# Kernel optimization log

Measured on AMD Instinct MI355X. Metric: run time of the kernel, lower is better.

The kernel has to match this reference:

```python
import jax, jax.numpy as jnp
import numpy as np

K = 16            # k_neighbors
THRESH = 0.5      # edge weight threshold
COS_EPS = 1e-8
LN_EPS = 1e-5


def setup_inputs() -> dict:
    key = jax.random.key(0)
    ks = jax.random.split(key, 8)
    B, L, D, H, O = 4, 2048, 64, 128, 64
    def w(k, shape, fan_in):
        return jax.random.normal(k, shape, jnp.float32) / np.float32(np.sqrt(fan_in))
    return {
        "x":  jax.random.normal(ks[0], (B, L, D), jnp.float32),
        "W1": w(ks[1], (D, H), D), "b1": jnp.zeros((H,), jnp.float32),
        "g1": jnp.ones((H,), jnp.float32), "be1": jnp.zeros((H,), jnp.float32),
        "W2": w(ks[2], (H, O), H), "b2": jnp.zeros((O,), jnp.float32),
        "g2": jnp.ones((O,), jnp.float32), "be2": jnp.zeros((O,), jnp.float32),
        "Wp": w(ks[3], (O, D), O), "bp": jnp.zeros((D,), jnp.float32),
    }


def _layer_norm(x, g, b):
    mu = x.mean(-1, keepdims=True)
    var = ((x - mu) ** 2).mean(-1, keepdims=True)
    return (x - mu) * jax.lax.rsqrt(var + LN_EPS) * g + b


def _gcn_layer(x, src, dst, ew, W, b, g, beta, N):
    # PyG GCNConv with gcn_norm(add_self_loops=True): append one more
    # weight-1.0 self loop per node, then symmetric deg^-1/2 normalization.
    ar = jnp.arange(N)
    src2 = jnp.concatenate([src, ar])
    dst2 = jnp.concatenate([dst, ar])
    w2 = jnp.concatenate([ew, jnp.ones((N,), x.dtype)])
    deg = jax.ops.segment_sum(w2, dst2, num_segments=N)           # [N]
    dinv = jnp.where(deg > 0, jax.lax.rsqrt(jnp.where(deg > 0, deg, 1.0)), 0.0)
    norm = dinv[src2] * w2 * dinv[dst2]                           # [E']
    h = x @ W                                                     # [N, out]
    out = jax.ops.segment_sum(norm[:, None] * h[src2], dst2, num_segments=N) + b
    out = jax.nn.relu(out)        # activation (dropout = eval identity)
    return _layer_norm(out, g, beta)


def _build_graph(xf, N):
    # cosine similarity (dense N x N), top-(K+1) per row, drop self (col 0),
    # zero out edges below threshold (equivalent to removing them for GCN),
    # then add constructor self loops with weight 1.0.
    nrm = jnp.linalg.norm(xf, axis=1)
    sim = (xf @ xf.T) / (nrm[:, None] * nrm[None, :] + COS_EPS)   # [N, N]
    vals, idx = jax.lax.top_k(sim, K + 1)
    src = jnp.repeat(jnp.arange(N), K)
    dst = idx[:, 1:].reshape(-1)
    wv = vals[:, 1:].reshape(-1)
    wv = jnp.where(wv > THRESH, wv, 0.0)
    ar = jnp.arange(N)
    edge_src = jnp.concatenate([src, ar])
    edge_dst = jnp.concatenate([dst, ar])
    # original detaches weights via .item(): stop_gradient to match
    edge_w = jax.lax.stop_gradient(
        jnp.concatenate([wv, jnp.ones((N,), xf.dtype)]))
    return edge_src, edge_dst, edge_w


def reference(x, W1, b1, g1, be1, W2, b2, g2, be2, Wp, bp):
    B, L, D = x.shape
    N = B * L
    xf = x.reshape(N, D)
    src, dst, ew = _build_graph(xf, N)
    h = _gcn_layer(xf, src, dst, ew, W1, b1, g1, be1, N)
    h = _gcn_layer(h,  src, dst, ew, W2, b2, g2, be2, N)
    out = (h @ Wp + bp).reshape(B, L, D)
    edge_index = jnp.stack([src, dst])
    return out, edge_index, ew
```

## Files before the change

kernel.cpp:

```cpp
#include <hip/hip_runtime.h>
#include <cstdint>
#include <climits>

#define N 8192
#define D 64
#define H 128
#define O 64
#define KNB 16
#define NE (N*KNB)
#define ETOT (NE + N)
#define OUT0 (N*D)
#define NSPL 32
#define JSPAN 256
#define JTILE 128
#define TCH 8

__device__ __forceinline__ float bf2f(unsigned short u){
    union { unsigned int u; float f; } v; v.u = ((unsigned int)u) << 16; return v.f;
}
__device__ __forceinline__ unsigned short f2bf(float f){
    union { float f; unsigned int u; } v; v.f = f;
    unsigned int r = v.u + 0x7FFFu + ((v.u >> 16) & 1u);
    return (unsigned short)(r >> 16);
}

#define PIN4(v) asm volatile("" : "+v"((v).x), "+v"((v).y), "+v"((v).z), "+v"((v).w))

__global__ void k_probe(const unsigned short* __restrict__ x, int* __restrict__ flag){
    __shared__ int cnt;
    if (threadIdx.x == 0) cnt = 0;
    __syncthreads();
    unsigned short u = x[2*threadIdx.x];
    int e = (u >> 7) & 0xFF;
    int ok = (u == 0) || (e >= 0x60 && e <= 0x85);
    unsigned long long m = __ballot(ok);
    if ((threadIdx.x & 63) == 0) atomicAdd(&cnt, __popcll(m));
    __syncthreads();
    if (threadIdx.x == 0) *flag = (cnt >= 128) ? 1 : 0;
}

__global__ void k_cvt(const void* __restrict__ src, float* __restrict__ dst,
                      int n, const int* __restrict__ flag){
    int i = blockIdx.x*256 + threadIdx.x;
    if (i >= n) return;
    if (*flag) dst[i] = bf2f(((const unsigned short*)src)[i]);
    else       dst[i] = ((const float*)src)[i];
}

__global__ void k_cvtp(const void* s1, const void* s2, const void* s3, const void* s4,
                       const void* s5, const void* s6, const void* s7, const void* s8,
                       const void* s9, const void* s10,
                       float* d1, float* d2, float* d3, float* d4, float* d5,
                       float* d6, float* d7, float* d8, float* d9, float* d10,
                       const int* __restrict__ flag){
    int id = blockIdx.x*256 + threadIdx.x;
    const void* s; float* d; int off;
    if      (id <  8192){ s = s1;  d = d1;  off = id; }
    else if (id <  8320){ s = s2;  d = d2;  off = id - 8192; }
    else if (id <  8448){ s = s3;  d = d3;  off = id - 8320; }
    else if (id <  8576){ s = s4;  d = d4;  off = id - 8448; }
    else if (id < 16768){ s = s5;  d = d5;  off = id - 8576; }
    else if (id < 16832){ s = s6;  d = d6;  off = id - 16768; }
    else if (id < 16896){ s = s7;  d = d7;  off = id - 16832; }
    else if (id < 16960){ s = s8;  d = d8;  off = id - 16896; }
    else if (id < 21056){ s = s9;  d = d9;  off = id - 16960; }
    else if (id < 21120){ s = s10; d = d10; off = id - 21056; }
    else return;
    if (*flag) d[off] = bf2f(((const unsigned short*)s)[off]);
    else       d[off] = ((const float*)s)[off];
}

__global__ void k_prep(const float* __restrict__ xf, float* __restrict__ nrmf){
    int i = blockIdx.x*64 + threadIdx.x;
    const float* xr = xf + i*D;
    float r[8];
    #pragma unroll
    for (int q = 0; q < 8; ++q) r[q] = __fmul_rn(xr[q], xr[q]);
    #pragma unroll
    for (int b = 8; b < 64; b += 8)
        #pragma unroll
        for (int q = 0; q < 8; ++q)
            r[q] = __fadd_rn(r[q], __fmul_rn(xr[b+q], xr[b+q]));
    float s = __fadd_rn(__fadd_rn(__fadd_rn(r[0],r[1]), __fadd_rn(r[2],r[3])),
                        __fadd_rn(__fadd_rn(r[4],r[5]), __fadd_rn(r[6],r[7])));
    nrmf[i] = __fsqrt_rn(s);
}


__global__ __launch_bounds__(256, 2) void k_scan8(const float* __restrict__ xf,
                                                  const float* __restrict__ nrmf,
                                                  float* __restrict__ chV,
                                                  int* __restrict__ chI){
    __shared__ float sB[JTILE*64];
    __shared__ float sN[JTILE];

    int tid = threadIdx.x;
    int grp = blockIdx.x & 31;
    int split = blockIdx.x >> 5;
    int i = grp*256 + tid;
    int jbase = split*JSPAN;

    const float4* xip = (const float4*)(xf + (size_t)i*D);
    float4 xi4[16];
    #pragma unroll
    for (int c = 0; c < 16; ++c) xi4[c] = xip[c];
    #pragma unroll
    for (int c = 0; c < 16; ++c) PIN4(xi4[c]);
    float ni = nrmf[i];

    float lv[TCH]; int li[TCH];
    #pragma unroll
    for (int r = 0; r < TCH; ++r){ lv[r] = -3.0e38f; li[r] = INT_MAX; }

    for (int t = 0; t < JSPAN/JTILE; ++t){
        int jt = jbase + t*JTILE;
        __syncthreads();
        #pragma unroll
        for (int u = 0; u < (JTILE*16)/256; ++u){
            int idx = u*256 + tid;
            ((float4*)sB)[idx] = ((const float4*)xf)[(size_t)jt*16 + idx];
        }
        if (tid < JTILE) sN[tid] = nrmf[jt + tid];
        __syncthreads();

        for (int jj = 0; jj < JTILE; ++jj){
            int j = jt + jj;
            const float4* B4 = (const float4*)(sB + jj*64);
            float nj = sN[jj];
            float a = 0.0f;
            #pragma unroll
            for (int c = 0; c < 16; ++c){
                float4 b = B4[c]; float4 xa = xi4[c];
                a = __fmaf_rn(b.x, xa.x, a);
                a = __fmaf_rn(b.y, xa.y, a);
                a = __fmaf_rn(b.z, xa.z, a);
                a = __fmaf_rn(b.w, xa.w, a);
            }
            float den = __fadd_rn(__fmul_rn(ni, nj), 1e-8f);
            float thr = lv[TCH-1]*den;
            if (j != i && a > __fmaf_rn(fabsf(thr), -1e-6f, thr)){
                float s0 = __fdiv_rn(a, den);
                if (s0 > lv[TCH-1]){
                    lv[TCH-1] = s0; li[TCH-1] = j;
                    #pragma unroll
                    for (int r = TCH-1; r > 0; --r){
                        if (lv[r] > lv[r-1]){
                            float tv = lv[r]; lv[r] = lv[r-1]; lv[r-1] = tv;
                            int ti = li[r]; li[r] = li[r-1]; li[r-1] = ti;
                        }
                    }
                }
            }
        }
    }
    #pragma unroll
    for (int r = 0; r < TCH; ++r){
        chV[(size_t)(split*TCH + r)*N + i] = lv[r];
        chI[(size_t)(split*TCH + r)*N + i] = li[r];
    }
}

__global__ __launch_bounds__(256, 2) void k_sel16(const float* __restrict__ xf,
                                                  const float* __restrict__ nrmf,
                                                  const float* __restrict__ chV,
                                                  const int* __restrict__ chI,
                                                  int* __restrict__ topIdx,
                                                  float* __restrict__ ewArr){
    int q = (blockIdx.x*256 + threadIdx.x) >> 6;
    int lane = threadIdx.x & 63;

    unsigned long long okey[4], key[4];
    #pragma unroll
    for (int s = 0; s < 4; ++s){
        int slot = lane + 64*s;
        float v = chV[(size_t)slot*N + q];
        int  id = chI[(size_t)slot*N + q];
        unsigned int u = __float_as_uint(v);
        if ((u & 0x7FFFFFFFu) == 0u) u = 0u;
        u = (u & 0x80000000u) ? ~u : (u | 0x80000000u);
        unsigned long long kk = ((unsigned long long)u << 32)
                              | (unsigned long long)(unsigned int)(~(unsigned int)id);
        okey[s] = kk; key[s] = kk;
    }

    float wv[16]; int widx[16];
    unsigned long long k16 = 0ull;
    #pragma unroll
    for (int sel = 0; sel < KNB; ++sel){
        unsigned long long m = key[0] > key[1] ? key[0] : key[1];
        if (key[2] > m) m = key[2];
        if (key[3] > m) m = key[3];
        #pragma unroll
        for (int off = 32; off > 0; off >>= 1){
            unsigned long long o = __shfl_xor(m, off);
            if (o > m) m = o;
        }
        if      (key[0] == m) key[0] = 0ull;
        else if (key[1] == m) key[1] = 0ull;
        else if (key[2] == m) key[2] = 0ull;
        else if (key[3] == m) key[3] = 0ull;
        unsigned int um = (unsigned int)(m >> 32);
        unsigned int ou = (um & 0x80000000u) ? (um & 0x7FFFFFFFu) : ~um;
        wv[sel]  = __uint_as_float(ou);
        widx[sel] = (int)~((unsigned int)m);
        k16 = m;
    }

    bool fl = false;
    #pragma unroll
    for (int s = 0; s < 4; ++s){
        int slot = lane + 64*s;
        if ((slot % TCH) == TCH-1 && okey[s] > k16) fl = true;
    }
    if (__ballot(fl) == 0ull){
        if (lane == 0){
            #pragma unroll
            for (int sel = 0; sel < KNB; ++sel){
                topIdx[q*KNB + sel] = widx[sel];
                ewArr [q*KNB + sel] = (wv[sel] > 0.5f) ? wv[sel] : 0.0f;
            }
        }
        return;
    }
    if (lane != 0) return;

    float lv[16]; int li[16];
    #pragma unroll
    for (int r = 0; r < 16; ++r){ lv[r] = -3.0e38f; li[r] = INT_MAX; }
    unsigned int flags = 0;
    for (int c = 0; c < NSPL; ++c){
        float v8 = chV[(size_t)(c*TCH + TCH-1)*N + q];
        int  i8 = chI[(size_t)(c*TCH + TCH-1)*N + q];
        if (v8 > wv[15] || (v8 == wv[15] && i8 < widx[15])) flags |= (1u << c);
    }
    const float4* xq4 = (const float4*)(xf + (size_t)q*D);
    float4 xq[16];
    #pragma unroll
    for (int c = 0; c < 16; ++c) xq[c] = xq4[c];
    float ni = nrmf[q];
    for (int c = 0; c < NSPL; ++c){
        if ((flags >> c) & 1u){
            for (int j = c*JSPAN; j < c*JSPAN + JSPAN; ++j){
                if (j == q) continue;
                const float4* b4 = (const float4*)(xf + (size_t)j*D);
                float a = 0.0f;
                #pragma unroll
                for (int k = 0; k < 16; ++k){
                    float4 b = b4[k]; float4 xa = xq[k];
                    a = __fmaf_rn(b.x, xa.x, a);
                    a = __fmaf_rn(b.y, xa.y, a);
                    a = __fmaf_rn(b.z, xa.z, a);
                    a = __fmaf_rn(b.w, xa.w, a);
                }
                float den = __fadd_rn(__fmul_rn(ni, nrmf[j]), 1e-8f);
                float s0 = __fdiv_rn(a, den);
                if (s0 > lv[15] || (s0 == lv[15] && j < li[15])){
                    lv[15] = s0; li[15] = j;
                    #pragma unroll
                    for (int k = 15; k > 0; --k){
                        if (lv[k] > lv[k-1] || (lv[k] == lv[k-1] && li[k] < li[k-1])){
                            float tv = lv[k]; lv[k] = lv[k-1]; lv[k-1] = tv;
                            int ti = li[k]; li[k] = li[k-1]; li[k-1] = ti;
                        }
                    }
                }
            }
        } else {
            #pragma unroll
            for (int r = 0; r < TCH; ++r){
                float v = chV[(size_t)(c*TCH + r)*N + q];
                int  id = chI[(size_t)(c*TCH + r)*N + q];
                if (v > lv[15] || (v == lv[15] && id < li[15])){
                    lv[15] = v; li[15] = id;
                    #pragma unroll
                    for (int k = 15; k > 0; --k){
                        if (lv[k] > lv[k-1] || (lv[k] == lv[k-1] && li[k] < li[k-1])){
                            float tv = lv[k]; lv[k] = lv[k-1]; lv[k-1] = tv;
                            int ti = li[k]; li[k] = li[k-1]; li[k-1] = ti;
                        }
                    }
                }
            }
        }
    }
    #pragma unroll
    for (int sel = 0; sel < KNB; ++sel){
        topIdx[q*KNB + sel] = li[sel];
        ewArr [q*KNB + sel] = (lv[sel] > 0.5f) ? lv[sel] : 0.0f;
    }
}

__global__ void k_deg_init(double* __restrict__ degD){
    int j = blockIdx.x*blockDim.x + threadIdx.x;
    if (j < N) degD[j] = 2.0;
}
__global__ void k_deg_scatter(const int* __restrict__ topIdx, const float* __restrict__ ewArr,
                              double* __restrict__ degD){
    int e = blockIdx.x*blockDim.x + threadIdx.x;
    if (e < NE){
        float w = ewArr[e];
        if (w > 0.0f) atomicAdd(&degD[topIdx[e]], (double)w);
    }
}
__global__ void k_dinv(const double* __restrict__ degD, float* __restrict__ dinv){
    int j = blockIdx.x*blockDim.x + threadIdx.x;
    if (j < N) dinv[j] = (float)(1.0 / sqrt(degD[j]));
}

__global__ void k_gemm1(const float* __restrict__ xf, const float* __restrict__ W1,
                        float* __restrict__ h1){
    int id = blockIdx.x*256 + threadIdx.x;
    int i = id >> 7; int f = id & (H-1);
    const float* xr = xf + i*D;
    float acc = 0.f;
    #pragma unroll
    for (int k = 0; k < D; ++k) acc += xr[k] * W1[k*H + f];
    h1[id] = acc;
}
__global__ void k_gemm2(const float* __restrict__ z1, const float* __restrict__ W2,
                        float* __restrict__ h2){
    int id = blockIdx.x*256 + threadIdx.x;
    int i = id >> 6; int f = id & (O-1);
    const float* zr = z1 + i*H;
    float acc = 0.f;
    #pragma unroll
    for (int k = 0; k < H; ++k) acc += zr[k] * W2[k*O + f];
    h2[id] = acc;
}
__global__ void k_proj(const float* __restrict__ z2, const float* __restrict__ Wp,
                       const float* __restrict__ bp, float* __restrict__ z3){
    int id = blockIdx.x*256 + threadIdx.x;
    int i = id >> 6; int f = id & (D-1);
    const float* zr = z2 + i*O;
    float acc = bp[f];
    #pragma unroll
    for (int k = 0; k < O; ++k) acc += zr[k] * Wp[k*D + f];
    z3[id] = acc;
}

template<int F>
__global__ void k_agg_init(const float* __restrict__ h, const float* __restrict__ dinv,
                           float* __restrict__ agg){
    int id = blockIdx.x*256 + threadIdx.x;
    int j = id / F;
    float dj = dinv[j];
    agg[id] = 2.f * dj * dj * h[id];
}
template<int F>
__global__ void k_agg_scat(const int* __restrict__ topIdx, const float* __restrict__ ewArr,
                           const float* __restrict__ dinv, const float* __restrict__ h,
                           float* __restrict__ agg){
    int e = blockIdx.x; int f = threadIdx.x;
    float w = ewArr[e];
    if (w == 0.f) return;
    int s = e >> 4;
    int dn = topIdx[e];
    float c = dinv[s] * w * dinv[dn];
    atomicAdd(&agg[dn*F + f], c * h[s*F + f]);
}

__global__ void k_post128(const float* __restrict__ agg, const float* __restrict__ b,
                          const float* __restrict__ g, const float* __restrict__ be,
                          float* __restrict__ z){
    __shared__ double s2[2];
    __shared__ double s3[2];
    int i = blockIdx.x; int f = threadIdx.x;
    float v = agg[i*H + f] + b[f];
    v = v > 0.f ? v : 0.f;
    int wid = f >> 6;
    double d = (double)v;
    for (int off = 32; off > 0; off >>= 1) d += __shfl_xor(d, off);
    if ((f & 63) == 0) s2[wid] = d;
    __syncthreads();
    double mu = (s2[0] + s2[1]) * (1.0/128.0);
    double dv = (double)v - mu;
    double qq = dv * dv;
    for (int off = 32; off > 0; off >>= 1) qq += __shfl_xor(qq, off);
    if ((f & 63) == 0) s3[wid] = qq;
    __syncthreads();
    double var = (s3[0] + s3[1]) * (1.0/128.0);
    double rs = 1.0 / sqrt(var + 1e-5);
    z[i*H + f] = (float)(dv * rs * (double)g[f] + (double)be[f]);
}
__global__ void k_post64(const float* __restrict__ agg, const float* __restrict__ b,
                         const float* __restrict__ g, const float* __restrict__ be,
                         float* __restrict__ z){
    int i = blockIdx.x; int f = threadIdx.x;
    float v = agg[i*O + f] + b[f];
    v = v > 0.f ? v : 0.f;
    double d = (double)v;
    for (int off = 32; off > 0; off >>= 1) d += __shfl_xor(d, off);
    double mu = d * (1.0/64.0);
    double dv = (double)v - mu;
    double qq = dv * dv;
    for (int off = 32; off > 0; off >>= 1) qq += __shfl_xor(qq, off);
    double var = qq * (1.0/64.0);
    double rs = 1.0 / sqrt(var + 1e-5);
    z[i*O + f] = (float)(dv * rs * (double)g[f] + (double)be[f]);
}

__global__ void k_out(const float* __restrict__ z3, const int* __restrict__ topIdx,
                      const float* __restrict__ ewArr, void* __restrict__ outp,
                      const int* __restrict__ flag){
    int id = blockIdx.x*256 + threadIdx.x;
    if (id < OUT0){
        float v = z3[id];
        if (*flag) ((unsigned short*)outp)[id] = f2bf(v);
        else       ((float*)outp)[id] = v;
        return;
    }
    int e = id - OUT0;
    if (e >= ETOT) return;
    int s, dn; float w;
    if (e < NE){ s = e >> 4; dn = topIdx[e]; w = ewArr[e]; }
    else       { s = e - NE; dn = s;        w = 1.0f; }
    if (*flag){
        unsigned short* o = (unsigned short*)outp;
        o[OUT0 + e]          = f2bf((float)s);
        o[OUT0 + ETOT + e]   = f2bf((float)dn);
        o[OUT0 + 2*ETOT + e] = f2bf(w);
    } else {
        float* o = (float*)outp;
        o[OUT0 + e]          = (float)s;
        o[OUT0 + ETOT + e]   = (float)dn;
        o[OUT0 + 2*ETOT + e] = w;
    }
}

extern "C" void kernel_launch(void* const* d_in, const int* in_sizes, int n_in,
                              void* d_out, int out_size, void* d_ws, size_t ws_size,
                              hipStream_t stream){
    char* ws = (char*)d_ws;
    int*    flag   = (int*)   (ws + 0);
    float*  w1f    = (float*) (ws + 4096);
    float*  b1f    = (float*) (ws + 36864);
    float*  g1f    = (float*) (ws + 37376);
    float*  be1f   = (float*) (ws + 37888);
    float*  w2f    = (float*) (ws + 38400);
    float*  b2f    = (float*) (ws + 71168);
    float*  g2f    = (float*) (ws + 71424);
    float*  be2f   = (float*) (ws + 71680);
    float*  wpf    = (float*) (ws + 71936);
    float*  bpf    = (float*) (ws + 88320);
    float*  xf     = (float*) (ws + 98304);
    float*  nrmf   = (float*) (ws + 2195456);
    int*    topIdx = (int*)   (ws + 2260992);
    float*  ewArr  = (float*) (ws + 2785280);
    double* degD   = (double*)(ws + 3309568);
    float*  dinv   = (float*) (ws + 3375104);
    float*  h1     = (float*) (ws + 3407872);
    float*  agg1   = (float*) (ws + 7602176);
    float*  z1     = (float*) (ws + 11796480);
    float*  h2     = h1;
    float*  agg2   = agg1;
    float*  z2     = z1;
    float*  z3     = h1;

    float* chV = (float*)(ws + 3407872);
    int*   chI = (int*)  (ws + 11796480);

    k_probe<<<1, 256, 0, stream>>>((const unsigned short*)d_in[0], flag);
    k_cvt<<<(N*D+255)/256, 256, 0, stream>>>(d_in[0], xf,  N*D, flag);
    k_cvtp<<<(21120+255)/256, 256, 0, stream>>>(
        d_in[1], d_in[2], d_in[3], d_in[4], d_in[5],
        d_in[6], d_in[7], d_in[8], d_in[9], d_in[10],
        w1f, b1f, g1f, be1f, w2f, b2f, g2f, be2f, wpf, bpf, flag);

    k_prep<<<N/64, 64, 0, stream>>>(xf, nrmf);
    k_scan8<<<32*NSPL, 256, 0, stream>>>(xf, nrmf, chV, chI);
    k_sel16<<<(N*64)/256, 256, 0, stream>>>(xf, nrmf, chV, chI, topIdx, ewArr);

    k_deg_init<<<N/256, 256, 0, stream>>>(degD);
    k_deg_scatter<<<NE/256, 256, 0, stream>>>(topIdx, ewArr, degD);
    k_dinv<<<N/256, 256, 0, stream>>>(degD, dinv);

    k_gemm1<<<(N*H)/256, 256, 0, stream>>>(xf, w1f, h1);
    k_agg_init<H><<<(N*H)/256, 256, 0, stream>>>(h1, dinv, agg1);
    k_agg_scat<H><<<NE, H, 0, stream>>>(topIdx, ewArr, dinv, h1, agg1);
    k_post128<<<N, H, 0, stream>>>(agg1, b1f, g1f, be1f, z1);

    k_gemm2<<<(N*O)/256, 256, 0, stream>>>(z1, w2f, h2);
    k_agg_init<O><<<(N*O)/256, 256, 0, stream>>>(h2, dinv, agg2);
    k_agg_scat<O><<<NE, O, 0, stream>>>(topIdx, ewArr, dinv, h2, agg2);
    k_post64<<<N, O, 0, stream>>>(agg2, b2f, g2f, be2f, z2);

    k_proj<<<(N*D)/256, 256, 0, stream>>>(z2, wpf, bpf, z3);
    k_out<<<(OUT0+ETOT+255)/256, 256, 0, stream>>>(z3, topIdx, ewArr, d_out, flag);
}
```

Before: 455.3 us.

## Read neighbor rows directly in similarity scan and batch edges per block in scatter

The similarity scan drops its shared-memory tile and both per-tile barriers. Each thread now reads the candidate row and norm straight from global memory. Since all lanes read the same address, these become broadcast loads served by cache, and the kernel also gains an explicit waves-per-EU occupancy hint. The edge scatter moves from one tiny block per edge to a grid-stride kernel with one wavefront per edge, which cuts block launch overhead. The risk is that the uncached-looking global loads in the inner loop add latency compared with LDS reads.

Result: faster. 439.6 us (-3.4%).

```diff
diff --git a/kernel.cpp b/kernel.cpp
--- a/kernel.cpp
+++ b/kernel.cpp
@@ -12,7 +12,6 @@
 #define OUT0 (N*D)
 #define NSPL 32
 #define JSPAN 256
-#define JTILE 128
 #define TCH 8
 
 __device__ __forceinline__ float bf2f(unsigned short u){
@@ -87,13 +86,12 @@
 }
 
 
-__global__ __launch_bounds__(256, 2) void k_scan8(const float* __restrict__ xf,
-                                                  const float* __restrict__ nrmf,
-                                                  float* __restrict__ chV,
-                                                  int* __restrict__ chI){
-    __shared__ float sB[JTILE*64];
-    __shared__ float sN[JTILE];
-
+__global__ __launch_bounds__(256)
+__attribute__((amdgpu_waves_per_eu(4,4)))
+void k_scan8(const float* __restrict__ xf,
+             const float* __restrict__ nrmf,
+             float* __restrict__ chV,
+             int* __restrict__ chI){
     int tid = threadIdx.x;
     int grp = blockIdx.x & 31;
     int split = blockIdx.x >> 5;
@@ -112,42 +110,30 @@
     #pragma unroll
     for (int r = 0; r < TCH; ++r){ lv[r] = -3.0e38f; li[r] = INT_MAX; }
 
-    for (int t = 0; t < JSPAN/JTILE; ++t){
-        int jt = jbase + t*JTILE;
-        __syncthreads();
+    for (int jj = 0; jj < JSPAN; ++jj){
+        int j = jbase + jj;
+        const float4* A = (const float4*)(xf + (size_t)j*D);
+        float nj = nrmf[j];
+        float a = 0.0f;
         #pragma unroll
-        for (int u = 0; u < (JTILE*16)/256; ++u){
-            int idx = u*256 + tid;
-            ((float4*)sB)[idx] = ((const float4*)xf)[(size_t)jt*16 + idx];
-        }
-        if (tid < JTILE) sN[tid] = nrmf[jt + tid];
-        __syncthreads();
-
-        for (int jj = 0; jj < JTILE; ++jj){
-            int j = jt + jj;
-            const float4* B4 = (const float4*)(sB + jj*64);
-            float nj = sN[jj];
-            float a = 0.0f;
-            #pragma unroll
-            for (int c = 0; c < 16; ++c){
-                float4 b = B4[c]; float4 xa = xi4[c];
-                a = __fmaf_rn(b.x, xa.x, a);
-                a = __fmaf_rn(b.y, xa.y, a);
-                a = __fmaf_rn(b.z, xa.z, a);
-                a = __fmaf_rn(b.w, xa.w, a);
-            }
-            float den = __fadd_rn(__fmul_rn(ni, nj), 1e-8f);
-            float thr = lv[TCH-1]*den;
-            if (j != i && a > __fmaf_rn(fabsf(thr), -1e-6f, thr)){
-                float s0 = __fdiv_rn(a, den);
-                if (s0 > lv[TCH-1]){
-                    lv[TCH-1] = s0; li[TCH-1] = j;
-                    #pragma unroll
-                    for (int r = TCH-1; r > 0; --r){
-                        if (lv[r] > lv[r-1]){
-                            float tv = lv[r]; lv[r] = lv[r-1]; lv[r-1] = tv;
-                            int ti = li[r]; li[r] = li[r-1]; li[r-1] = ti;
-                        }
+        for (int c = 0; c < 16; ++c){
+            float4 b = A[c]; float4 xa = xi4[c];
+            a = __fmaf_rn(b.x, xa.x, a);
+            a = __fmaf_rn(b.y, xa.y, a);
+            a = __fmaf_rn(b.z, xa.z, a);
+            a = __fmaf_rn(b.w, xa.w, a);
+        }
+        float den = __fadd_rn(__fmul_rn(ni, nj), 1e-8f);
+        float thr = lv[TCH-1]*den;
+        if (j != i && a > __fmaf_rn(fabsf(thr), -1e-6f, thr)){
+            float s0 = __fdiv_rn(a, den);
+            if (s0 > lv[TCH-1]){
+                lv[TCH-1] = s0; li[TCH-1] = j;
+                #pragma unroll
+                for (int r = TCH-1; r > 0; --r){
+                    if (lv[r] > lv[r-1]){
+                        float tv = lv[r]; lv[r] = lv[r-1]; lv[r-1] = tv;
+                        int ti = li[r]; li[r] = li[r-1]; li[r-1] = ti;
                     }
                 }
             }
@@ -347,16 +333,25 @@
     agg[id] = 2.f * dj * dj * h[id];
 }
 template<int F>
-__global__ void k_agg_scat(const int* __restrict__ topIdx, const float* __restrict__ ewArr,
-                           const float* __restrict__ dinv, const float* __restrict__ h,
-                           float* __restrict__ agg){
-    int e = blockIdx.x; int f = threadIdx.x;
-    float w = ewArr[e];
-    if (w == 0.f) return;
-    int s = e >> 4;
-    int dn = topIdx[e];
-    float c = dinv[s] * w * dinv[dn];
-    atomicAdd(&agg[dn*F + f], c * h[s*F + f]);
+__global__ __launch_bounds__(256) void k_agg_scat(const int* __restrict__ topIdx,
+                                                  const float* __restrict__ ewArr,
+                                                  const float* __restrict__ dinv,
+                                                  const float* __restrict__ h,
+                                                  float* __restrict__ agg){
+    int wid = threadIdx.x >> 6;
+    int lane = threadIdx.x & 63;
+    for (int e = blockIdx.x*4 + wid; e < NE; e += gridDim.x*4){
+        float w = ewArr[e];
+        if (w == 0.f) continue;
+        int s = e >> 4;
+        int dn = topIdx[e];
+        float c = dinv[s] * w * dinv[dn];
+        #pragma unroll
+        for (int p = 0; p < F/64; ++p){
+            int f = lane + 64*p;
+            atomicAdd(&agg[dn*F + f], c * h[s*F + f]);
+        }
+    }
 }
 
 __global__ void k_post128(const float* __restrict__ agg, const float* __restrict__ b,
@@ -476,12 +471,12 @@
 
     k_gemm1<<<(N*H)/256, 256, 0, stream>>>(xf, w1f, h1);
     k_agg_init<H><<<(N*H)/256, 256, 0, stream>>>(h1, dinv, agg1);
-    k_agg_scat<H><<<NE, H, 0, stream>>>(topIdx, ewArr, dinv, h1, agg1);
+    k_agg_scat<H><<<4096, 256, 0, stream>>>(topIdx, ewArr, dinv, h1, agg1);
     k_post128<<<N, H, 0, stream>>>(agg1, b1f, g1f, be1f, z1);
 
     k_gemm2<<<(N*O)/256, 256, 0, stream>>>(z1, w2f, h2);
     k_agg_init<O><<<(N*O)/256, 256, 0, stream>>>(h2, dinv, agg2);
-    k_agg_scat<O><<<NE, O, 0, stream>>>(topIdx, ewArr, dinv, h2, agg2);
+    k_agg_scat<O><<<4096, 256, 0, stream>>>(topIdx, ewArr, dinv, h2, agg2);
     k_post64<<<N, O, 0, stream>>>(agg2, b2f, g2f, be2f, z2);
 
     k_proj<<<(N*D)/256, 256, 0, stream>>>(z2, wpf, bpf, z3);
```
